# Kernel tuning notes

Measured on AMD Instinct MI355X. Metric: run time of the kernel, lower is better.

Reference implementation:

```python
import jax, jax.numpy as jnp
import numpy as np

D_IN = 4097   # 4096 obj feat + 1 depth
D_H1 = 512
D_H2 = 256
N_HEADS = 4
D_HEAD = D_H2 // N_HEADS
D_FF = 512


def setup_inputs() -> dict:
    key = jax.random.key(0)
    ks = jax.random.split(key, 20)
    B, T, N = 2, 100, 30
    s = lambda *sh: 1.0 / np.sqrt(sh[0])
    inp = {
        "object_features": jax.random.normal(ks[0], (B, T, N, 4096), jnp.float32),
        "object_depths": jax.random.uniform(ks[1], (B, T, N, 1), jnp.float32),
        # spatial encoder (2-layer fully-connected message passing)
        "W1a": jax.random.normal(ks[2], (D_IN, D_H1), jnp.float32) * s(D_IN),
        "W2a": jax.random.normal(ks[3], (D_IN, D_H1), jnp.float32) * s(D_IN),
        "b1a": jnp.zeros((D_H1,), jnp.float32),
        "W1b": jax.random.normal(ks[4], (D_H1, D_H2), jnp.float32) * s(D_H1),
        "W2b": jax.random.normal(ks[5], (D_H1, D_H2), jnp.float32) * s(D_H1),
        "b1b": jnp.zeros((D_H2,), jnp.float32),
        # temporal transformer encoder layer (post-LN)
        "Wq": jax.random.normal(ks[6], (D_H2, D_H2), jnp.float32) * s(D_H2),
        "Wk": jax.random.normal(ks[7], (D_H2, D_H2), jnp.float32) * s(D_H2),
        "Wv": jax.random.normal(ks[8], (D_H2, D_H2), jnp.float32) * s(D_H2),
        "Wo": jax.random.normal(ks[9], (D_H2, D_H2), jnp.float32) * s(D_H2),
        "ln1_g": jnp.ones((D_H2,), jnp.float32),
        "ln1_b": jnp.zeros((D_H2,), jnp.float32),
        "Wf1": jax.random.normal(ks[10], (D_H2, D_FF), jnp.float32) * s(D_H2),
        "bf1": jnp.zeros((D_FF,), jnp.float32),
        "Wf2": jax.random.normal(ks[11], (D_FF, D_H2), jnp.float32) * s(D_FF),
        "bf2": jnp.zeros((D_H2,), jnp.float32),
        "ln2_g": jnp.ones((D_H2,), jnp.float32),
        "ln2_b": jnp.zeros((D_H2,), jnp.float32),
        # classifier
        "Wc": jax.random.normal(ks[12], (D_H2, 1), jnp.float32) * s(D_H2),
        "bc": jnp.zeros((1,), jnp.float32),
    }
    return inp


def _layer_norm(x, g, b, eps=1e-5):
    mu = jnp.mean(x, axis=-1, keepdims=True)
    var = jnp.var(x, axis=-1, keepdims=True)
    return (x - mu) * jax.lax.rsqrt(var + eps) * g + b


def _forward(object_features, object_depths, W1a, W2a, b1a, W1b, W2b, b1b,
             Wq, Wk, Wv, Wo, ln1_g, ln1_b, Wf1, bf1, Wf2, bf2, ln2_g, ln2_b,
             Wc, bc):
    B, T, N, _ = object_features.shape
    x = jnp.concatenate([object_features, object_depths], axis=-1)  # (B,T,N,4097)
    # fully-connected graph (torch.combinations, both directions):
    # aggregated message for node i = mean over all j != i.
    def mp(h, Ws, Wn, b):
        neigh = (jnp.sum(h, axis=2, keepdims=True) - h) / (N - 1)
        return jax.nn.relu(h @ Ws + neigh @ Wn + b)
    h = mp(x, W1a, W2a, b1a)      # (B,T,N,512)
    h = mp(h, W1b, W2b, b1b)      # (B,T,N,256)
    g = jnp.mean(h, axis=2)       # global mean pool -> (B,T,256)
    # temporal transformer encoder (self-attention over T, post-LN)
    q = (g @ Wq).reshape(B, T, N_HEADS, D_HEAD)
    k = (g @ Wk).reshape(B, T, N_HEADS, D_HEAD)
    v = (g @ Wv).reshape(B, T, N_HEADS, D_HEAD)
    scores = jnp.einsum("bthd,bshd->bhts", q, k) / np.sqrt(D_HEAD)
    attn = jax.nn.softmax(scores, axis=-1)
    ctx = jnp.einsum("bhts,bshd->bthd", attn, v).reshape(B, T, D_H2) @ Wo
    y = _layer_norm(g + ctx, ln1_g, ln1_b)
    ff = jax.nn.relu(y @ Wf1 + bf1) @ Wf2 + bf2
    z = _layer_norm(y + ff, ln2_g, ln2_b)  # (B,T,256)
    # dropout is identity in eval mode -> probs2 == probs, uncertainty == 0
    logits = (z @ Wc + bc).squeeze(-1)     # (B,T)
    probs = jax.nn.sigmoid(logits)
    uncertainty = jnp.zeros_like(probs)
    return probs, uncertainty


def reference(object_features, object_depths, W1a, W2a, b1a, W1b, W2b, b1b,
              Wq, Wk, Wv, Wo, ln1_g, ln1_b, Wf1, bf1, Wf2, bf2, ln2_g, ln2_b,
              Wc, bc):
    return _forward(object_features, object_depths, W1a, W2a, b1a, W1b, W2b,
                    b1b, Wq, Wk, Wv, Wo, ln1_g, ln1_b, Wf1, bf1, Wf2, bf2,
                    ln2_g, ln2_b, Wc, bc)
```

## Files before the change

kernel.cpp:

```cpp
#include <hip/hip_runtime.h>
#include <hip/hip_bf16.h>
#include <stdint.h>

typedef unsigned short u16;
typedef __attribute__((ext_vector_type(8))) short short8;
typedef __attribute__((ext_vector_type(4))) float floatx4;
typedef __attribute__((ext_vector_type(4))) unsigned short ushort4_t;

#define BT 200
#define NOBJ 30
#define KPAD 4160
#define DIN 4097
#define DH1 512
#define DH2 256
#define DFF 512
#define MPAD 6016
#define SPAD 256
#define NKB (KPAD / 32)
#define NBIG (NKB * (DH1/32))

__device__ __forceinline__ u16 f2bf(float f) {
    union { float f; uint32_t u; } c; c.f = f;
    uint32_t u = c.u;
    u += 0x7FFF + ((u >> 16) & 1);
    return (u16)(u >> 16);
}
__device__ __forceinline__ float bf2f(u16 h) {
    union { uint32_t u; float f; } c; c.u = ((uint32_t)h) << 16;
    return c.f;
}

__device__ __forceinline__ void load16_lds(const u16* g, u16* l) {
    __builtin_amdgcn_global_load_lds(
        (const __attribute__((address_space(1))) void*)g,
        (__attribute__((address_space(3))) void*)l, 16, 0, 0);
}

__global__ void prep(const float* __restrict__ W1a, const float* __restrict__ W2a,
                     const float* __restrict__ W1b, const float* __restrict__ W2b,
                     u16* __restrict__ Wc1T, u16* __restrict__ W2aTs,
                     u16* __restrict__ Wc2T, u16* __restrict__ W2bTs) {
    __shared__ float t1[32][33];
    __shared__ float t2[32][33];
    int bid = blockIdx.x;
    if (bid < NBIG) {
        int kb = (bid % NKB) * 32, jb = (bid / NKB) * 32;
        int tx = threadIdx.x & 31, ty = threadIdx.x >> 5;
        #pragma unroll
        for (int r = 0; r < 32; r += 8) {
            int k = kb + ty + r, j = jb + tx;
            float a = 0.f, b = 0.f;
            if (k < DIN) { a = W1a[k * DH1 + j]; b = W2a[k * DH1 + j]; }
            float bs = b * (1.f / 29.f);
            t1[ty + r][tx] = a - bs;
            t2[ty + r][tx] = bs;
        }
        __syncthreads();
        #pragma unroll
        for (int r = 0; r < 32; r += 8) {
            int j = jb + ty + r, k = kb + tx;
            Wc1T[(size_t)j * KPAD + k]  = f2bf(t1[tx][ty + r]);
            W2aTs[(size_t)j * KPAD + k] = f2bf(t2[tx][ty + r]);
        }
    } else {
        int idx = (bid - NBIG) * 256 + threadIdx.x;
        int j = idx >> 9, k = idx & 511;
        float a = W1b[k * DH2 + j];
        float b = W2b[k * DH2 + j] * (1.f / 29.f);
        Wc2T[j * DH1 + k]  = f2bf(a - b);
        W2bTs[j * DH1 + k] = f2bf(b);
    }
}

__global__ void sum_convert(const float* __restrict__ feat, const float* __restrict__ depth,
                            u16* __restrict__ Xb, u16* __restrict__ Sb) {
    int bt = blockIdx.x;
    int k = (blockIdx.y * 256 + threadIdx.x) * 4;
    if (k >= KPAD) return;
    float s0 = 0.f, s1 = 0.f, s2 = 0.f, s3 = 0.f;
    for (int n = 0; n < NOBJ; n++) {
        float4 v;
        if (k + 3 < 4096) {
            v = *(const float4*)(feat + (size_t)(bt * NOBJ + n) * 4096 + k);
        } else {
            v.x = (k == 4096) ? depth[bt * NOBJ + n] : 0.f;
            v.y = 0.f; v.z = 0.f; v.w = 0.f;
        }
        s0 += v.x; s1 += v.y; s2 += v.z; s3 += v.w;
        ushort4_t o; o.x = f2bf(v.x); o.y = f2bf(v.y); o.z = f2bf(v.z); o.w = f2bf(v.w);
        *(ushort4_t*)(Xb + (size_t)(bt * NOBJ + n) * KPAD + k) = o;
    }
    ushort4_t so; so.x = f2bf(s0); so.y = f2bf(s1); so.z = f2bf(s2); so.w = f2bf(s3);
    *(ushort4_t*)(Sb + (size_t)bt * KPAD + k) = so;
}

__global__ __launch_bounds__(256) void gemm128(
    const u16* __restrict__ A, const u16* __restrict__ B,
    int M, int N, int K, int kiters, int mode,
    const float* __restrict__ row_add, int row_div,
    const float* __restrict__ col_add,
    float* __restrict__ outF) {
    __shared__ __align__(16) u16 Al[128 * 64];
    __shared__ __align__(16) u16 Bl[128 * 64];
    int tid = threadIdx.x;
    int lane = tid & 63, w = tid >> 6;
    int n0 = blockIdx.x * 128, m0 = blockIdx.y * 128;
    int kbeg = blockIdx.z * kiters * 64;
    int kend = min(K, kbeg + kiters * 64);

    int srow = tid >> 3, kslot = tid & 7;
    floatx4 acc[4][4] = {};
    int lrow = lane & 15, q = lane >> 4;
    int wm = (w & 1) * 64, wn = (w >> 1) * 64;
    int swzbase = lrow & 7;

    for (int kb = kbeg; kb < kend; kb += 64) {
        #pragma unroll
        for (int it = 0; it < 4; it++) {
            int row = it * 32 + srow;
            int kph = kslot ^ (row & 7);
            load16_lds(A + (size_t)(m0 + row) * K + kb + kph * 8,
                       Al + it * 2048 + w * 512);
            load16_lds(B + (size_t)(n0 + row) * K + kb + kph * 8,
                       Bl + it * 2048 + w * 512);
        }
        __syncthreads();
        #pragma unroll
        for (int h = 0; h < 2; h++) {
            int ci = h * 4 + q;
            int so = (ci ^ swzbase) * 8;
            short8 af[4], bfv[4];
            #pragma unroll
            for (int i = 0; i < 4; i++)
                af[i] = *(short8*)(Al + (wm + i * 16 + lrow) * 64 + so);
            #pragma unroll
            for (int j = 0; j < 4; j++)
                bfv[j] = *(short8*)(Bl + (wn + j * 16 + lrow) * 64 + so);
            #pragma unroll
            for (int i = 0; i < 4; i++)
                #pragma unroll
                for (int j = 0; j < 4; j++)
                    acc[i][j] = __builtin_amdgcn_mfma_f32_16x16x32_bf16(af[i], bfv[j], acc[i][j], 0, 0, 0);
        }
        __syncthreads();
    }

    #pragma unroll
    for (int i = 0; i < 4; i++) {
        #pragma unroll
        for (int j = 0; j < 4; j++) {
            #pragma unroll
            for (int r = 0; r < 4; r++) {
                int row = m0 + wm + i * 16 + q * 4 + r;
                int col = n0 + wn + j * 16 + lrow;
                if (row < M) {
                    float v = acc[i][j][r];
                    if (mode == 0) {
                        atomicAdd(&outF[(size_t)row * N + col], v);
                    } else {
                        v += row_add[(row / row_div) * N + col] + col_add[col];
                        v = v > 0.f ? v : 0.f;
                        outF[(size_t)row * N + col] = v;
                    }
                }
            }
        }
    }
}

__global__ __launch_bounds__(256) void gemm64(
    const u16* __restrict__ A, const u16* __restrict__ B,
    int M, int N, int K, int kiters,
    float* __restrict__ outAcc) {
    __shared__ __align__(16) u16 Al[64 * 64];
    __shared__ __align__(16) u16 Bl[128 * 64];
    int tid = threadIdx.x;
    int lane = tid & 63, w = tid >> 6;
    int n0 = blockIdx.x * 128, m0 = blockIdx.y * 64;
    int kbeg = blockIdx.z * kiters * 64;
    int kend = min(K, kbeg + kiters * 64);

    int srow = tid >> 3, kslot = tid & 7;
    floatx4 acc[2][4] = {};
    int lrow = lane & 15, q = lane >> 4;
    int wm = (w & 1) * 32, wn = (w >> 1) * 64;
    int swzbase = lrow & 7;

    for (int kb = kbeg; kb < kend; kb += 64) {
        #pragma unroll
        for (int it = 0; it < 2; it++) {
            int row = it * 32 + srow;
            int kph = kslot ^ (row & 7);
            load16_lds(A + (size_t)(m0 + row) * K + kb + kph * 8,
                       Al + it * 2048 + w * 512);
        }
        #pragma unroll
        for (int it = 0; it < 4; it++) {
            int row = it * 32 + srow;
            int kph = kslot ^ (row & 7);
            load16_lds(B + (size_t)(n0 + row) * K + kb + kph * 8,
                       Bl + it * 2048 + w * 512);
        }
        __syncthreads();
        #pragma unroll
        for (int h = 0; h < 2; h++) {
            int ci = h * 4 + q;
            int so = (ci ^ swzbase) * 8;
            short8 af[2], bfv[4];
            #pragma unroll
            for (int i = 0; i < 2; i++)
                af[i] = *(short8*)(Al + (wm + i * 16 + lrow) * 64 + so);
            #pragma unroll
            for (int j = 0; j < 4; j++)
                bfv[j] = *(short8*)(Bl + (wn + j * 16 + lrow) * 64 + so);
            #pragma unroll
            for (int i = 0; i < 2; i++)
                #pragma unroll
                for (int j = 0; j < 4; j++)
                    acc[i][j] = __builtin_amdgcn_mfma_f32_16x16x32_bf16(af[i], bfv[j], acc[i][j], 0, 0, 0);
        }
        __syncthreads();
    }

    #pragma unroll
    for (int i = 0; i < 2; i++) {
        #pragma unroll
        for (int j = 0; j < 4; j++) {
            #pragma unroll
            for (int r = 0; r < 4; r++) {
                int row = m0 + wm + i * 16 + q * 4 + r;
                int col = n0 + wn + j * 16 + lrow;
                if (row < M)
                    atomicAdd(&outAcc[(size_t)row * N + col], acc[i][j][r]);
            }
        }
    }
}

__global__ void reduce1(const float* __restrict__ hacc, const float* __restrict__ u,
                        const float* __restrict__ b1a,
                        u16* __restrict__ hb, u16* __restrict__ Shb) {
    __shared__ float sl[128];
    int bt = blockIdx.x, c0 = blockIdx.y * 128;
    int lc = threadIdx.x & 127, rp = threadIdx.x >> 7;
    int col = c0 + lc;
    float ub = u[bt * DH1 + col] + b1a[col];
    float s = 0.f;
    for (int n = rp; n < NOBJ; n += 2) {
        float v = hacc[(size_t)(bt * NOBJ + n) * DH1 + col] + ub;
        v = v > 0.f ? v : 0.f;
        hb[(size_t)(bt * NOBJ + n) * DH1 + col] = f2bf(v);
        s += v;
    }
    if (rp == 0) sl[lc] = s;
    __syncthreads();
    if (rp == 1) Shb[bt * DH1 + col] = f2bf(sl[lc] + s);
}

__global__ void reduce2_qkv(const float* __restrict__ h2,
                            const float* __restrict__ Wq, const float* __restrict__ Wk,
                            const float* __restrict__ Wv,
                            float* __restrict__ g, float* __restrict__ q,
                            float* __restrict__ k, float* __restrict__ v) {
    __shared__ float gl[DH2];
    int bt = blockIdx.x, j = threadIdx.x;
    float a = 0.f;
    for (int n = 0; n < NOBJ; n++)
        a += h2[(size_t)(bt * NOBJ + n) * DH2 + j];
    a *= (1.f / 30.f);
    gl[j] = a;
    g[bt * DH2 + j] = a;
    __syncthreads();
    float aq = 0.f, ak = 0.f, av = 0.f;
    for (int kk = 0; kk < DH2; kk++) {
        float x = gl[kk];
        aq += x * Wq[kk * DH2 + j];
        ak += x * Wk[kk * DH2 + j];
        av += x * Wv[kk * DH2 + j];
    }
    q[bt * DH2 + j] = aq;
    k[bt * DH2 + j] = ak;
    v[bt * DH2 + j] = av;
}

__device__ __forceinline__ float block_sum256(float v, volatile float* red) {
    #pragma unroll
    for (int o = 32; o > 0; o >>= 1) v += __shfl_down(v, o);
    int w = threadIdx.x >> 6;
    __syncthreads();
    if ((threadIdx.x & 63) == 0) red[w] = v;
    __syncthreads();
    return red[0] + red[1] + red[2] + red[3];
}

__global__ void attn_head(const float* __restrict__ qg, const float* __restrict__ kg,
                          const float* __restrict__ vg, const float* __restrict__ g,
                          const float* __restrict__ Wo,
                          const float* __restrict__ ln1g, const float* __restrict__ ln1b,
                          const float* __restrict__ Wf1, const float* __restrict__ bf1,
                          const float* __restrict__ Wf2, const float* __restrict__ bf2,
                          const float* __restrict__ ln2g, const float* __restrict__ ln2b,
                          const float* __restrict__ Wc, const float* __restrict__ bc,
                          float* __restrict__ out) {
    __shared__ float ql[DH2];
    __shared__ float scl[4][128];
    __shared__ float ctxl[DH2];
    __shared__ float yl[DH2];
    __shared__ float ffl[DFF];
    __shared__ float red[4];
    int row = blockIdx.x, tid = threadIdx.x;
    int b = (row >= 100) ? 1 : 0;
    int base = b * 100;
    ql[tid] = qg[row * DH2 + tid];
    __syncthreads();

    for (int p = tid; p < 512; p += 256) {
        int h = p >> 7, s = p & 127;
        if (s < 100) {
            const float* kr = kg + (size_t)(base + s) * DH2 + h * 64;
            float a = 0.f;
            #pragma unroll 8
            for (int d = 0; d < 64; d++) a += ql[h * 64 + d] * kr[d];
            scl[h][s] = a * 0.125f;
        }
    }
    __syncthreads();

    {
        int w = tid >> 6, lane = tid & 63;
        int s2 = 64 + lane;
        float a  = scl[w][lane];
        float b2 = (s2 < 100) ? scl[w][s2] : -1e30f;
        float m = fmaxf(a, b2);
        #pragma unroll
        for (int o = 32; o > 0; o >>= 1) m = fmaxf(m, __shfl_down(m, o));
        m = __shfl(m, 0);
        float e1 = __expf(a - m);
        float e2 = (s2 < 100) ? __expf(b2 - m) : 0.f;
        float sm = e1 + e2;
        #pragma unroll
        for (int o = 32; o > 0; o >>= 1) sm += __shfl_down(sm, o);
        sm = __shfl(sm, 0);
        float r = 1.f / sm;
        scl[w][lane] = e1 * r;
        if (s2 < 100) scl[w][s2] = e2 * r;
    }
    __syncthreads();

    {
        int h = tid >> 6;
        float o = 0.f;
        for (int s = 0; s < 100; s++)
            o += scl[h][s] * vg[(size_t)(base + s) * DH2 + tid];
        ctxl[tid] = o;
    }
    __syncthreads();

    float o = 0.f;
    for (int kk = 0; kk < DH2; kk++) o += ctxl[kk] * Wo[kk * DH2 + tid];
    float t = g[row * DH2 + tid] + o;
    float mu  = block_sum256(t, red) * (1.f / DH2);
    float ex2 = block_sum256(t * t, red) * (1.f / DH2);
    float y = (t - mu) * rsqrtf(ex2 - mu * mu + 1e-5f) * ln1g[tid] + ln1b[tid];
    yl[tid] = y;
    __syncthreads();
    for (int jj = tid; jj < DFF; jj += 256) {
        float a = bf1[jj];
        for (int kk = 0; kk < DH2; kk++) a += yl[kk] * Wf1[kk * DFF + jj];
        ffl[jj] = a > 0.f ? a : 0.f;
    }
    __syncthreads();
    float o2 = bf2[tid];
    for (int kk = 0; kk < DFF; kk++) o2 += ffl[kk] * Wf2[kk * DH2 + tid];
    float z0 = y + o2;
    float mu2  = block_sum256(z0, red) * (1.f / DH2);
    float ex22 = block_sum256(z0 * z0, red) * (1.f / DH2);
    float z = (z0 - mu2) * rsqrtf(ex22 - mu2 * mu2 + 1e-5f) * ln2g[tid] + ln2b[tid];
    float logit = block_sum256(z * Wc[tid], red) + bc[0];
    if (tid == 0) {
        out[row]      = 1.f / (1.f + __expf(-logit));
        out[BT + row] = 0.f;
    }
}

extern "C" void kernel_launch(void* const* d_in, const int* in_sizes, int n_in,
                              void* d_out, int out_size, void* d_ws, size_t ws_size,
                              hipStream_t stream) {
    const float* feat  = (const float*)d_in[0];
    const float* depth = (const float*)d_in[1];
    const float* W1a = (const float*)d_in[2];
    const float* W2a = (const float*)d_in[3];
    const float* b1a = (const float*)d_in[4];
    const float* W1b = (const float*)d_in[5];
    const float* W2b = (const float*)d_in[6];
    const float* b1b = (const float*)d_in[7];
    const float* Wq  = (const float*)d_in[8];
    const float* Wk  = (const float*)d_in[9];
    const float* Wv  = (const float*)d_in[10];
    const float* Wo  = (const float*)d_in[11];
    const float* ln1g = (const float*)d_in[12];
    const float* ln1b = (const float*)d_in[13];
    const float* Wf1 = (const float*)d_in[14];
    const float* bf1 = (const float*)d_in[15];
    const float* Wf2 = (const float*)d_in[16];
    const float* bf2 = (const float*)d_in[17];
    const float* ln2g = (const float*)d_in[18];
    const float* ln2b = (const float*)d_in[19];
    const float* Wc  = (const float*)d_in[20];
    const float* bc  = (const float*)d_in[21];
    float* out = (float*)d_out;
    char* ws = (char*)d_ws;

    size_t off = 0;
    u16* Xb    = (u16*)(ws + off); off += (size_t)MPAD * KPAD * 2;
    u16* Sb    = (u16*)(ws + off); off += (size_t)SPAD * KPAD * 2;
    u16* Wc1T  = (u16*)(ws + off); off += (size_t)DH1 * KPAD * 2;
    u16* W2aTs = (u16*)(ws + off); off += (size_t)DH1 * KPAD * 2;
    u16* Wc2T  = (u16*)(ws + off); off += (size_t)DH2 * DH1 * 2;
    u16* W2bTs = (u16*)(ws + off); off += (size_t)DH2 * DH1 * 2;
    u16* hb    = (u16*)(ws + off); off += (size_t)MPAD * DH1 * 2;
    u16* Shb   = (u16*)(ws + off); off += (size_t)SPAD * DH1 * 2;
    char* zBase = ws + off;
    float* hacc = (float*)(ws + off); off += (size_t)6000 * DH1 * 4;
    float* u    = (float*)(ws + off); off += (size_t)BT * DH1 * 4;
    float* u2   = (float*)(ws + off); off += (size_t)BT * DH2 * 4;
    size_t zBytes = (size_t)(ws + off - zBase);
    float* g   = (float*)(ws + off); off += (size_t)BT * DH2 * 4;
    float* q   = (float*)(ws + off); off += (size_t)BT * DH2 * 4;
    float* k   = (float*)(ws + off); off += (size_t)BT * DH2 * 4;
    float* v   = (float*)(ws + off); off += (size_t)BT * DH2 * 4;
    float* h2  = (float*)Xb;

    hipMemsetAsync(zBase, 0, zBytes, stream);
    prep<<<NBIG + 512, 256, 0, stream>>>(W1a, W2a, W1b, W2b, Wc1T, W2aTs, Wc2T, W2bTs);
    sum_convert<<<dim3(BT, 5), 256, 0, stream>>>(feat, depth, Xb, Sb);

    gemm64<<<dim3(4, 4, 6), 256, 0, stream>>>(Sb, W2aTs, BT, DH1, KPAD, 11, u);
    gemm128<<<dim3(4, 47, 2), 256, 0, stream>>>(Xb, Wc1T, 6000, DH1, KPAD, 33, 0,
                                                nullptr, 1, nullptr, hacc);
    reduce1<<<dim3(BT, 4), 256, 0, stream>>>(hacc, u, b1a, hb, Shb);
    gemm64<<<dim3(2, 4, 2), 256, 0, stream>>>(Shb, W2bTs, BT, DH2, DH1, 4, u2);
    gemm128<<<dim3(2, 47, 1), 256, 0, stream>>>(hb, Wc2T, 6000, DH2, DH1, 8, 1,
                                                u2, NOBJ, b1b, h2);
    reduce2_qkv<<<BT, DH2, 0, stream>>>(h2, Wq, Wk, Wv, g, q, k, v);
    attn_head<<<BT, DH2, 0, stream>>>(q, k, v, g, Wo, ln1g, ln1b, Wf1, bf1,
                                      Wf2, bf2, ln2g, ln2b, Wc, bc, out);
}
```

Baseline: 407.5 us.

## Merge prep kernels and paired GEMMs into single launches with split-K rebalancing

```diff
diff --git a/kernel.cpp b/kernel.cpp
--- a/kernel.cpp
+++ b/kernel.cpp
@@ -18,6 +18,8 @@
 #define SPAD 256
 #define NKB (KPAD / 32)
 #define NBIG (NKB * (DH1/32))
+#define NSMALL 512
+#define NCONV 1000
 
 __device__ __forceinline__ u16 f2bf(float f) {
     union { float f; uint32_t u; } c; c.f = f;
@@ -36,10 +38,12 @@
         (__attribute__((address_space(3))) void*)l, 16, 0, 0);
 }
 
-__global__ void prep(const float* __restrict__ W1a, const float* __restrict__ W2a,
-                     const float* __restrict__ W1b, const float* __restrict__ W2b,
-                     u16* __restrict__ Wc1T, u16* __restrict__ W2aTs,
-                     u16* __restrict__ Wc2T, u16* __restrict__ W2bTs) {
+__global__ void prep_all(const float* __restrict__ W1a, const float* __restrict__ W2a,
+                         const float* __restrict__ W1b, const float* __restrict__ W2b,
+                         const float* __restrict__ feat, const float* __restrict__ depth,
+                         u16* __restrict__ Wc1T, u16* __restrict__ W2aTs,
+                         u16* __restrict__ Wc2T, u16* __restrict__ W2bTs,
+                         u16* __restrict__ Xb, u16* __restrict__ Sb) {
     __shared__ float t1[32][33];
     __shared__ float t2[32][33];
     int bid = blockIdx.x;
@@ -62,52 +66,61 @@
             Wc1T[(size_t)j * KPAD + k]  = f2bf(t1[tx][ty + r]);
             W2aTs[(size_t)j * KPAD + k] = f2bf(t2[tx][ty + r]);
         }
-    } else {
+    } else if (bid < NBIG + NSMALL) {
         int idx = (bid - NBIG) * 256 + threadIdx.x;
         int j = idx >> 9, k = idx & 511;
         float a = W1b[k * DH2 + j];
         float b = W2b[k * DH2 + j] * (1.f / 29.f);
         Wc2T[j * DH1 + k]  = f2bf(a - b);
         W2bTs[j * DH1 + k] = f2bf(b);
-    }
-}
-
-__global__ void sum_convert(const float* __restrict__ feat, const float* __restrict__ depth,
-                            u16* __restrict__ Xb, u16* __restrict__ Sb) {
-    int bt = blockIdx.x;
-    int k = (blockIdx.y * 256 + threadIdx.x) * 4;
-    if (k >= KPAD) return;
-    float s0 = 0.f, s1 = 0.f, s2 = 0.f, s3 = 0.f;
-    for (int n = 0; n < NOBJ; n++) {
-        float4 v;
-        if (k + 3 < 4096) {
-            v = *(const float4*)(feat + (size_t)(bt * NOBJ + n) * 4096 + k);
-        } else {
-            v.x = (k == 4096) ? depth[bt * NOBJ + n] : 0.f;
-            v.y = 0.f; v.z = 0.f; v.w = 0.f;
-        }
-        s0 += v.x; s1 += v.y; s2 += v.z; s3 += v.w;
-        ushort4_t o; o.x = f2bf(v.x); o.y = f2bf(v.y); o.z = f2bf(v.z); o.w = f2bf(v.w);
-        *(ushort4_t*)(Xb + (size_t)(bt * NOBJ + n) * KPAD + k) = o;
-    }
-    ushort4_t so; so.x = f2bf(s0); so.y = f2bf(s1); so.z = f2bf(s2); so.w = f2bf(s3);
-    *(ushort4_t*)(Sb + (size_t)bt * KPAD + k) = so;
-}
-
-__global__ __launch_bounds__(256) void gemm128(
-    const u16* __restrict__ A, const u16* __restrict__ B,
-    int M, int N, int K, int kiters, int mode,
-    const float* __restrict__ row_add, int row_div,
-    const float* __restrict__ col_add,
-    float* __restrict__ outF) {
+    } else {
+        int cid = bid - NBIG - NSMALL;
+        int bt = cid / 5;
+        int k = ((cid % 5) * 256 + threadIdx.x) * 4;
+        if (k >= KPAD) return;
+        float s0 = 0.f, s1 = 0.f, s2 = 0.f, s3 = 0.f;
+        for (int n = 0; n < NOBJ; n++) {
+            float4 v;
+            if (k + 3 < 4096) {
+                v = *(const float4*)(feat + (size_t)(bt * NOBJ + n) * 4096 + k);
+            } else {
+                v.x = (k == 4096) ? depth[bt * NOBJ + n] : 0.f;
+                v.y = 0.f; v.z = 0.f; v.w = 0.f;
+            }
+            s0 += v.x; s1 += v.y; s2 += v.z; s3 += v.w;
+            ushort4_t o; o.x = f2bf(v.x); o.y = f2bf(v.y); o.z = f2bf(v.z); o.w = f2bf(v.w);
+            *(ushort4_t*)(Xb + (size_t)(bt * NOBJ + n) * KPAD + k) = o;
+        }
+        ushort4_t so; so.x = f2bf(s0); so.y = f2bf(s1); so.z = f2bf(s2); so.w = f2bf(s3);
+        *(ushort4_t*)(Sb + (size_t)bt * KPAD + k) = so;
+    }
+}
+
+__global__ __launch_bounds__(256) void gemmA(
+    const u16* __restrict__ Xb, const u16* __restrict__ Wc1T,
+    const u16* __restrict__ Sb, const u16* __restrict__ W2aTs,
+    float* __restrict__ hacc, float* __restrict__ uOut) {
     __shared__ __align__(16) u16 Al[128 * 64];
     __shared__ __align__(16) u16 Bl[128 * 64];
+    int bid = blockIdx.x;
+    const u16 *A, *B;
+    float* outF;
+    int m0, n0, kbeg, kend, M;
+    if (bid < 564) {
+        int x = bid & 3, y = (bid >> 2) % 47, z = bid / 188;
+        A = Xb; B = Wc1T; outF = hacc; M = 6000;
+        m0 = y * 128; n0 = x * 128;
+        kbeg = z * 22 * 64; kend = min(KPAD, kbeg + 22 * 64);
+    } else {
+        int rem = bid - 564;
+        int x = rem & 3, y = (rem >> 2) & 1, z = rem >> 3;
+        A = Sb; B = W2aTs; outF = uOut; M = BT;
+        m0 = y * 128; n0 = x * 128;
+        kbeg = z * 11 * 64; kend = min(KPAD, kbeg + 11 * 64);
+    }
+    const int N = DH1;
     int tid = threadIdx.x;
     int lane = tid & 63, w = tid >> 6;
-    int n0 = blockIdx.x * 128, m0 = blockIdx.y * 128;
-    int kbeg = blockIdx.z * kiters * 64;
-    int kend = min(K, kbeg + kiters * 64);
-
     int srow = tid >> 3, kslot = tid & 7;
     floatx4 acc[4][4] = {};
     int lrow = lane & 15, q = lane >> 4;
@@ -119,9 +132,9 @@
         for (int it = 0; it < 4; it++) {
             int row = it * 32 + srow;
             int kph = kslot ^ (row & 7);
-            load16_lds(A + (size_t)(m0 + row) * K + kb + kph * 8,
+            load16_lds(A + (size_t)(m0 + row) * KPAD + kb + kph * 8,
                        Al + it * 2048 + w * 512);
-            load16_lds(B + (size_t)(n0 + row) * K + kb + kph * 8,
+            load16_lds(B + (size_t)(n0 + row) * KPAD + kb + kph * 8,
                        Bl + it * 2048 + w * 512);
         }
         __syncthreads();
@@ -146,40 +159,42 @@
     }
 
     #pragma unroll
-    for (int i = 0; i < 4; i++) {
-        #pragma unroll
-        for (int j = 0; j < 4; j++) {
+    for (int i = 0; i < 4; i++)
+        #pragma unroll
+        for (int j = 0; j < 4; j++)
             #pragma unroll
             for (int r = 0; r < 4; r++) {
                 int row = m0 + wm + i * 16 + q * 4 + r;
                 int col = n0 + wn + j * 16 + lrow;
-                if (row < M) {
-                    float v = acc[i][j][r];
-                    if (mode == 0) {
-                        atomicAdd(&outF[(size_t)row * N + col], v);
-                    } else {
-                        v += row_add[(row / row_div) * N + col] + col_add[col];
-                        v = v > 0.f ? v : 0.f;
-                        outF[(size_t)row * N + col] = v;
-                    }
-                }
+                if (row < M)
+                    atomicAdd(&outF[(size_t)row * N + col], acc[i][j][r]);
             }
-        }
-    }
-}
-
-__global__ __launch_bounds__(256) void gemm64(
-    const u16* __restrict__ A, const u16* __restrict__ B,
-    int M, int N, int K, int kiters,
-    float* __restrict__ outAcc) {
+}
+
+__global__ __launch_bounds__(256) void gemmB(
+    const u16* __restrict__ hb, const u16* __restrict__ Wc2T,
+    const u16* __restrict__ Shb, const u16* __restrict__ W2bTs,
+    float* __restrict__ hacc2, float* __restrict__ u2Out) {
     __shared__ __align__(16) u16 Al[64 * 64];
     __shared__ __align__(16) u16 Bl[128 * 64];
+    int bid = blockIdx.x;
+    const u16 *A, *B;
+    float* outF;
+    int m0, n0, kbeg, M;
+    if (bid < 376) {
+        int x = bid & 1, y = (bid >> 1) % 94, z = bid / 188;
+        A = hb; B = Wc2T; outF = hacc2; M = 6000;
+        m0 = y * 64; n0 = x * 128; kbeg = z * 4 * 64;
+    } else {
+        int rem = bid - 376;
+        int x = rem & 1, y = (rem >> 1) & 3, z = rem >> 3;
+        A = Shb; B = W2bTs; outF = u2Out; M = BT;
+        m0 = y * 64; n0 = x * 128; kbeg = z * 4 * 64;
+    }
+    int kend = kbeg + 4 * 64;
+    const int N = DH2, K = DH1;
     int tid = threadIdx.x;
     int lane = tid & 63, w = tid >> 6;
-    int n0 = blockIdx.x * 128, m0 = blockIdx.y * 64;
-    int kbeg = blockIdx.z * kiters * 64;
-    int kend = min(K, kbeg + kiters * 64);
-
     int srow = tid >> 3, kslot = tid & 7;
     floatx4 acc[2][4] = {};
     int lrow = lane & 15, q = lane >> 4;
@@ -223,18 +238,16 @@
     }
 
     #pragma unroll
-    for (int i = 0; i < 2; i++) {
-        #pragma unroll
-        for (int j = 0; j < 4; j++) {
+    for (int i = 0; i < 2; i++)
+        #pragma unroll
+        for (int j = 0; j < 4; j++)
             #pragma unroll
             for (int r = 0; r < 4; r++) {
                 int row = m0 + wm + i * 16 + q * 4 + r;
                 int col = n0 + wn + j * 16 + lrow;
                 if (row < M)
-                    atomicAdd(&outAcc[(size_t)row * N + col], acc[i][j][r]);
+                    atomicAdd(&outF[(size_t)row * N + col], acc[i][j][r]);
             }
-        }
-    }
 }
 
 __global__ void reduce1(const float* __restrict__ hacc, const float* __restrict__ u,
@@ -257,16 +270,20 @@
     if (rp == 1) Shb[bt * DH1 + col] = f2bf(sl[lc] + s);
 }
 
-__global__ void reduce2_qkv(const float* __restrict__ h2,
+__global__ void reduce2_qkv(const float* __restrict__ hacc2, const float* __restrict__ u2,
+                            const float* __restrict__ b1b,
                             const float* __restrict__ Wq, const float* __restrict__ Wk,
                             const float* __restrict__ Wv,
                             float* __restrict__ g, float* __restrict__ q,
                             float* __restrict__ k, float* __restrict__ v) {
     __shared__ float gl[DH2];
     int bt = blockIdx.x, j = threadIdx.x;
+    float ub = u2[bt * DH2 + j] + b1b[j];
     float a = 0.f;
-    for (int n = 0; n < NOBJ; n++)
-        a += h2[(size_t)(bt * NOBJ + n) * DH2 + j];
+    for (int n = 0; n < NOBJ; n++) {
+        float vv = hacc2[(size_t)(bt * NOBJ + n) * DH2 + j] + ub;
+        a += vv > 0.f ? vv : 0.f;
+    }
     a *= (1.f / 30.f);
     gl[j] = a;
     g[bt * DH2 + j] = a;
@@ -309,8 +326,7 @@
     __shared__ float ffl[DFF];
     __shared__ float red[4];
     int row = blockIdx.x, tid = threadIdx.x;
-    int b = (row >= 100) ? 1 : 0;
-    int base = b * 100;
+    int base = (row >= 100) ? 100 : 0;
     ql[tid] = qg[row * DH2 + tid];
     __syncthreads();
 
@@ -421,28 +437,23 @@
     u16* hb    = (u16*)(ws + off); off += (size_t)MPAD * DH1 * 2;
     u16* Shb   = (u16*)(ws + off); off += (size_t)SPAD * DH1 * 2;
     char* zBase = ws + off;
-    float* hacc = (float*)(ws + off); off += (size_t)6000 * DH1 * 4;
-    float* u    = (float*)(ws + off); off += (size_t)BT * DH1 * 4;
-    float* u2   = (float*)(ws + off); off += (size_t)BT * DH2 * 4;
+    float* hacc  = (float*)(ws + off); off += (size_t)6000 * DH1 * 4;
+    float* hacc2 = (float*)(ws + off); off += (size_t)6000 * DH2 * 4;
+    float* u     = (float*)(ws + off); off += (size_t)SPAD * DH1 * 4;
+    float* u2    = (float*)(ws + off); off += (size_t)SPAD * DH2 * 4;
     size_t zBytes = (size_t)(ws + off - zBase);
     float* g   = (float*)(ws + off); off += (size_t)BT * DH2 * 4;
     float* q   = (float*)(ws + off); off += (size_t)BT * DH2 * 4;
     float* k   = (float*)(ws + off); off += (size_t)BT * DH2 * 4;
     float* v   = (float*)(ws + off); off += (size_t)BT * DH2 * 4;
-    float* h2  = (float*)Xb;
 
     hipMemsetAsync(zBase, 0, zBytes, stream);
-    prep<<<NBIG + 512, 256, 0, stream>>>(W1a, W2a, W1b, W2b, Wc1T, W2aTs, Wc2T, W2bTs);
-    sum_convert<<<dim3(BT, 5), 256, 0, stream>>>(feat, depth, Xb, Sb);
-
-    gemm64<<<dim3(4, 4, 6), 256, 0, stream>>>(Sb, W2aTs, BT, DH1, KPAD, 11, u);
-    gemm128<<<dim3(4, 47, 2), 256, 0, stream>>>(Xb, Wc1T, 6000, DH1, KPAD, 33, 0,
-                                                nullptr, 1, nullptr, hacc);
+    prep_all<<<NBIG + NSMALL + NCONV, 256, 0, stream>>>(
+        W1a, W2a, W1b, W2b, feat, depth, Wc1T, W2aTs, Wc2T, W2bTs, Xb, Sb);
+    gemmA<<<564 + 48, 256, 0, stream>>>(Xb, Wc1T, Sb, W2aTs, hacc, u);
     reduce1<<<dim3(BT, 4), 256, 0, stream>>>(hacc, u, b1a, hb, Shb);
-    gemm64<<<dim3(2, 4, 2), 256, 0, stream>>>(Shb, W2bTs, BT, DH2, DH1, 4, u2);
-    gemm128<<<dim3(2, 47, 1), 256, 0, stream>>>(hb, Wc2T, 6000, DH2, DH1, 8, 1,
-                                                u2, NOBJ, b1b, h2);
-    reduce2_qkv<<<BT, DH2, 0, stream>>>(h2, Wq, Wk, Wv, g, q, k, v);
+    gemmB<<<376 + 16, 256, 0, stream>>>(hb, Wc2T, Shb, W2bTs, hacc2, u2);
+    reduce2_qkv<<<BT, DH2, 0, stream>>>(hacc2, u2, b1b, Wq, Wk, Wv, g, q, k, v);
     attn_head<<<BT, DH2, 0, stream>>>(q, k, v, g, Wo, ln1g, ln1b, Wf1, bf1,
                                       Wf2, bf2, ln2g, ln2b, Wc, bc, out);
 }
```

Measured after the change: 398.6 us. 1.02x faster.
